# Kernel optimization log

Hardware: AMD Instinct MI355X
Metric: run time of the kernel (lower is better)

Reference implementation:

```python
import jax, jax.numpy as jnp
import numpy as np

GROUPS = 32
GN_EPS = 1e-6


def setup_inputs() -> dict:
    key = jax.random.key(0)
    ks = jax.random.split(key, 6)
    B, C, H, W = 2, 512, 64, 64
    s = 1.0 / np.sqrt(C)
    return {
        "x": jax.random.normal(ks[0], (B, C, H, W), jnp.float32),
        "gamma": jnp.ones((C,), jnp.float32),
        "beta": jnp.zeros((C,), jnp.float32),
        "wq": jax.random.normal(ks[1], (C, C), jnp.float32) * s,
        "bq": jnp.zeros((C,), jnp.float32),
        "wk": jax.random.normal(ks[2], (C, C), jnp.float32) * s,
        "bk": jnp.zeros((C,), jnp.float32),
        "wv": jax.random.normal(ks[3], (C, C), jnp.float32) * s,
        "bv": jnp.zeros((C,), jnp.float32),
        "wp": jax.random.normal(ks[4], (C, C), jnp.float32) * s,
        "bp": jnp.zeros((C,), jnp.float32),
    }


def _group_norm(x, gamma, beta):
    B, C, H, W = x.shape
    xg = x.reshape(B, GROUPS, C // GROUPS, H, W)
    mean = jnp.mean(xg, axis=(2, 3, 4), keepdims=True)
    var = jnp.mean(jnp.square(xg - mean), axis=(2, 3, 4), keepdims=True)
    xn = ((xg - mean) * jax.lax.rsqrt(var + GN_EPS)).reshape(B, C, H, W)
    return xn * gamma[None, :, None, None] + beta[None, :, None, None]


def _conv1x1(x, w, b):
    # 1x1 conv == per-pixel linear over channels; w: [out, in]
    return jnp.einsum('oc,bchw->bohw', w, x) + b[None, :, None, None]


def reference(x, gamma, beta, wq, bq, wk, bk, wv, bv, wp, bp):
    B, C, H, W = x.shape
    N = H * W
    h = _group_norm(x, gamma, beta)
    q = _conv1x1(h, wq, bq).reshape(B, C, N)  # [B, C, N]
    k = _conv1x1(h, wk, bk).reshape(B, C, N)
    v = _conv1x1(h, wv, bv).reshape(B, C, N)
    scale = C ** (-0.5)
    # attn[b, i, j] = softmax_j(q_i . k_j * scale)
    scores = jnp.einsum('bci,bcj->bij', q, k) * scale
    attn = jax.nn.softmax(scores, axis=2)
    # out[b, c, i] = sum_j attn[b, i, j] * v[b, c, j]
    o = jnp.einsum('bij,bcj->bci', attn, v).reshape(B, C, H, W)
    o = _conv1x1(o, wp, bp)
    return x + o
```

## Files before the change

kernel.cpp:

```cpp
#include <hip/hip_runtime.h>
#include <hip/hip_bf16.h>

using bf16 = __hip_bfloat16;
typedef __attribute__((ext_vector_type(4))) float f32x4;
typedef __attribute__((ext_vector_type(8))) short bf16x8;

#define NPX 4096
#define CCH 512

struct Ptr8 { void* p[8]; };

struct GemmP {
  const bf16* A; const bf16* B; void* C;
  const float* bias_m; const float* bias_n; const float* resid;
  float* rspart;
  float alpha; int K;
  int lda, ldb, ldc;
  long long sA, sB, sC, sR;
  int gx, gy;
  int omode;
};

__device__ __forceinline__ void async16(const bf16* g, bf16* l) {
  __builtin_amdgcn_global_load_lds((const __attribute__((address_space(1))) void*)g,
                                   (__attribute__((address_space(3))) void*)l, 16, 0, 0);
}

__device__ __forceinline__ float bfb2f(short s) {
  unsigned u = ((unsigned)(unsigned short)s) << 16;
  float f;
  __builtin_memcpy(&f, &u, 4);
  return f;
}

__device__ __forceinline__ short f2bfb(float f) {
  bf16 h = __float2bfloat16(f);
  short s;
  __builtin_memcpy(&s, &h, 2);
  return s;
}

__global__ __launch_bounds__(256) void prep_kernel(
    const float* __restrict__ wq, const float* __restrict__ wk,
    const float* __restrict__ wv, const float* __restrict__ wp,
    const float* __restrict__ bq, const float* __restrict__ bk,
    const float* __restrict__ x,
    bf16* __restrict__ wout, float* __restrict__ bqk, float* __restrict__ pstats) {
  int bid = blockIdx.x;
  int t = threadIdx.x;
  if (bid < 1024) {
    int tid = bid * 256 + t;
    int i = tid * 4;
    int seg = i >> 18;
    const float* in = seg == 0 ? wq : seg == 1 ? wk : seg == 2 ? wv : wp;
    float4 v = *reinterpret_cast<const float4*>(in + (i & 262143));
    wout[i]     = __float2bfloat16(v.x);
    wout[i + 1] = __float2bfloat16(v.y);
    wout[i + 2] = __float2bfloat16(v.z);
    wout[i + 3] = __float2bfloat16(v.w);
    if (tid < 256) {
      int j = tid * 4;
      const float* bsrc = j < 512 ? bq : bk;
      float4 b = *reinterpret_cast<const float4*>(bsrc + (j & 511));
      *reinterpret_cast<float4*>(bqk + j) = b;
    }
  } else {
    int bp = bid - 1024;
    const float* p = x + (size_t)bp * 8192;
    float s = 0.f, s2 = 0.f;
    #pragma unroll
    for (int j = 0; j < 8; j++) {
      float4 v = *reinterpret_cast<const float4*>(p + j * 1024 + t * 4);
      s  += v.x + v.y + v.z + v.w;
      s2 += v.x * v.x + v.y * v.y + v.z * v.z + v.w * v.w;
    }
    #pragma unroll
    for (int off = 32; off >= 1; off >>= 1) {
      s  += __shfl_xor(s, off);
      s2 += __shfl_xor(s2, off);
    }
    __shared__ float ls[8];
    int wv_ = t >> 6;
    if ((t & 63) == 0) { ls[wv_ * 2] = s; ls[wv_ * 2 + 1] = s2; }
    __syncthreads();
    if (t == 0) {
      pstats[bp * 2]     = ls[0] + ls[2] + ls[4] + ls[6];
      pstats[bp * 2 + 1] = ls[1] + ls[3] + ls[5] + ls[7];
    }
  }
}

__global__ __launch_bounds__(256) void gn_apply_kernel(const float* __restrict__ x,
    const float* __restrict__ pstats, const float* __restrict__ gamma,
    const float* __restrict__ beta, bf16* __restrict__ h) {
  __shared__ float tile[64][65];
  __shared__ float mr[4][2];
  int b  = blockIdx.z;
  int c0 = blockIdx.x * 64, n0 = blockIdx.y * 64;
  int t  = threadIdx.x;
  if (t < 4) {
    int g = (c0 >> 4) + t;
    float S = 0.f, S2 = 0.f;
    #pragma unroll
    for (int k2 = 0; k2 < 8; k2++) {
      S  += pstats[((b * 32 + g) * 8 + k2) * 2];
      S2 += pstats[((b * 32 + g) * 8 + k2) * 2 + 1];
    }
    float mean = S * (1.f / 65536.f);
    float var  = S2 * (1.f / 65536.f) - mean * mean;
    mr[t][0] = mean;
    mr[t][1] = rsqrtf(var + 1e-6f);
  }
  __syncthreads();
  int cl = t >> 6, nl = t & 63;
  #pragma unroll
  for (int i = 0; i < 16; i++) {
    int c = c0 + cl + i * 4;
    float v = x[((size_t)b * CCH + c) * NPX + n0 + nl];
    int gi = (cl + i * 4) >> 4;
    tile[cl + i * 4][nl] = (v - mr[gi][0]) * mr[gi][1] * gamma[c] + beta[c];
  }
  __syncthreads();
  #pragma unroll
  for (int i = 0; i < 16; i++) {
    int n = cl + i * 4;
    int c = nl;
    h[((size_t)b * NPX + n0 + n) * CCH + c0 + c] = __float2bfloat16(tile[c][n]);
  }
}

__global__ __launch_bounds__(256, 4) void gemm_any_kernel(GemmP p0, GemmP p1, unsigned nb0) {
  unsigned nwg = gridDim.x;
  unsigned flat = blockIdx.x;
  unsigned swz = (flat & 7) * (nwg >> 3) + (flat >> 3);
  GemmP p = swz < nb0 ? p0 : p1;
  unsigned local = swz < nb0 ? swz : swz - nb0;
  unsigned bxi = local % p.gx;
  unsigned tmp = local / p.gx;
  unsigned byi = tmp % p.gy;
  unsigned bz  = tmp / p.gy;

  const bf16* A = p.A + (size_t)bz * p.sA;
  const bf16* B = p.B + (size_t)bz * p.sB;
  const int m0 = bxi * 128, n0 = byi * 128;

  __shared__ bf16 ldsA[128 * 64];
  __shared__ bf16 ldsB[128 * 64];

  const int t = threadIdx.x;
  const int lane = t & 63, wv = t >> 6;
  const int wr = (wv >> 1) * 64, wc = (wv & 1) * 64;

  const int r0 = t >> 3;
  const int cb = ((t & 7) << 4) ^ ((r0 & 7) << 4);
  const bf16* gA = A + (size_t)(m0 + r0) * p.lda + (cb >> 1);
  const bf16* gB = B + (size_t)(n0 + r0) * p.ldb + (cb >> 1);
  bf16* lA = ldsA + t * 8;
  bf16* lB = ldsB + t * 8;

  const int arow = wr + (lane & 15);
  const int brow = wc + (lane & 15);
  const int kb   = (lane >> 4) * 16;

  f32x4 acc[4][4] = {};

  for (int k0 = 0; k0 < p.K; k0 += 64) {
    #pragma unroll
    for (int i = 0; i < 4; i++) {
      async16(gA + (size_t)i * 32 * p.lda + k0, lA + i * 2048);
      async16(gB + (size_t)i * 32 * p.ldb + k0, lB + i * 2048);
    }
    __syncthreads();
    #pragma unroll
    for (int ks = 0; ks < 2; ks++) {
      bf16x8 af[4], bfr[4];
      #pragma unroll
      for (int f = 0; f < 4; f++) {
        int ra = arow + f * 16;
        af[f] = *reinterpret_cast<const bf16x8*>(
            reinterpret_cast<const char*>(ldsA) + ra * 128 + ((ks * 64 + kb) ^ ((ra & 7) << 4)));
        int rb = brow + f * 16;
        bfr[f] = *reinterpret_cast<const bf16x8*>(
            reinterpret_cast<const char*>(ldsB) + rb * 128 + ((ks * 64 + kb) ^ ((rb & 7) << 4)));
      }
      #pragma unroll
      for (int fm = 0; fm < 4; fm++)
        #pragma unroll
        for (int fn = 0; fn < 4; fn++)
          acc[fm][fn] = __builtin_amdgcn_mfma_f32_16x16x32_bf16(af[fm], bfr[fn], acc[fm][fn], 0, 0, 0);
    }
    __syncthreads();
  }

  #pragma unroll
  for (int fm = 0; fm < 4; fm++) {
    #pragma unroll
    for (int j = 0; j < 4; j++) {
      int gm = m0 + wr + fm * 16 + (lane >> 4) * 4 + j;
      if (p.omode == 2) {
        float rsum = 0.f;
        #pragma unroll
        for (int fn = 0; fn < 4; fn++) {
          int gn = n0 + wc + fn * 16 + (lane & 15);
          float e = __expf(acc[fm][fn][j] * p.alpha);
          rsum += e;
          reinterpret_cast<bf16*>(p.C)[(size_t)bz * p.sC + (size_t)gm * p.ldc + gn] = __float2bfloat16(e);
        }
        rsum += __shfl_xor(rsum, 1);
        rsum += __shfl_xor(rsum, 2);
        rsum += __shfl_xor(rsum, 4);
        rsum += __shfl_xor(rsum, 8);
        if ((lane & 15) == 0)
          p.rspart[(((size_t)bz * 4096 + gm) << 6) + byi * 2 + (wv & 1)] = rsum;
      } else {
        float bm = p.bias_m ? p.bias_m[gm] : 0.f;
        #pragma unroll
        for (int fn = 0; fn < 4; fn++) {
          int gn = n0 + wc + fn * 16 + (lane & 15);
          float vv = acc[fm][fn][j] * p.alpha + bm;
          if (p.bias_n) vv += p.bias_n[gn];
          if (p.resid)  vv += p.resid[(size_t)bz * p.sR + (size_t)gm * p.ldc + gn];
          if (p.omode == 1)
            reinterpret_cast<bf16*>(p.C)[(size_t)bz * p.sC + (size_t)gm * p.ldc + gn] = __float2bfloat16(vv);
          else
            reinterpret_cast<float*>(p.C)[(size_t)bz * p.sC + (size_t)gm * p.ldc + gn] = vv;
        }
      }
    }
  }
}

__global__ __launch_bounds__(256, 4) void pv_split_kernel(
    const bf16* __restrict__ Sb, const bf16* __restrict__ vb,
    const float* __restrict__ rspart,
    long long sS, long long sV, Ptr8 slots, int mode) {
  unsigned nx = gridDim.x, ny = gridDim.y;
  unsigned flat = (blockIdx.z * ny + blockIdx.y) * nx + blockIdx.x;
  unsigned nwg = nx * ny * gridDim.z;
  unsigned swz = (flat & 7) * (nwg >> 3) + (flat >> 3);
  unsigned bxi = swz % nx;
  unsigned tmp = swz / nx;
  unsigned byi = tmp % ny;
  unsigned bz  = tmp / ny;

  const int z = bz;
  const int b = mode ? 0 : (z >> 2);
  const int s = mode ? z : (z & 3);
  const bf16* A = Sb + (size_t)b * sS + s * 1024;
  const bf16* B = vb + (size_t)b * sV + s * 1024;
  bf16* Cp = (bf16*)(slots.p[z]);
  const int m0 = bxi * 128, n0 = byi * 128;

  __shared__ bf16 ldsA[128 * 64];
  __shared__ bf16 ldsB[128 * 64];
  __shared__ float rs_lds[128];

  const int t = threadIdx.x;

  if (t < 128) {
    const float4* pp = reinterpret_cast<const float4*>(rspart + (((size_t)b * 4096 + m0 + t) << 6));
    float ssum = 0.f;
    #pragma unroll
    for (int i2 = 0; i2 < 16; i2++) {
      float4 vv = pp[i2];
      ssum += vv.x + vv.y + vv.z + vv.w;
    }
    rs_lds[t] = 1.0f / ssum;
  }

  const int lane = t & 63, wv = t >> 6;
  const int wr = (wv >> 1) * 64, wc = (wv & 1) * 64;

  const int r0 = t >> 3;
  const int cb = ((t & 7) << 4) ^ ((r0 & 7) << 4);
  const bf16* gA = A + (size_t)(m0 + r0) * 4096 + (cb >> 1);
  const bf16* gB = B + (size_t)(n0 + r0) * 4096 + (cb >> 1);
  bf16* lA = ldsA + t * 8;
  bf16* lB = ldsB + t * 8;

  const int arow = wr + (lane & 15);
  const int brow = wc + (lane & 15);
  const int kb   = (lane >> 4) * 16;

  f32x4 acc[4][4] = {};

  for (int k0 = 0; k0 < 1024; k0 += 64) {
    #pragma unroll
    for (int i = 0; i < 4; i++) {
      async16(gA + (size_t)i * 32 * 4096 + k0, lA + i * 2048);
      async16(gB + (size_t)i * 32 * 4096 + k0, lB + i * 2048);
    }
    __syncthreads();
    #pragma unroll
    for (int ks = 0; ks < 2; ks++) {
      bf16x8 af[4], bfr[4];
      #pragma unroll
      for (int f = 0; f < 4; f++) {
        int ra = arow + f * 16;
        af[f] = *reinterpret_cast<const bf16x8*>(
            reinterpret_cast<const char*>(ldsA) + ra * 128 + ((ks * 64 + kb) ^ ((ra & 7) << 4)));
        int rb = brow + f * 16;
        bfr[f] = *reinterpret_cast<const bf16x8*>(
            reinterpret_cast<const char*>(ldsB) + rb * 128 + ((ks * 64 + kb) ^ ((rb & 7) << 4)));
      }
      #pragma unroll
      for (int fm = 0; fm < 4; fm++)
        #pragma unroll
        for (int fn = 0; fn < 4; fn++)
          acc[fm][fn] = __builtin_amdgcn_mfma_f32_16x16x32_bf16(af[fm], bfr[fn], acc[fm][fn], 0, 0, 0);
    }
    __syncthreads();
  }

  #pragma unroll
  for (int fm = 0; fm < 4; fm++) {
    #pragma unroll
    for (int j = 0; j < 4; j++) {
      int lrow = wr + fm * 16 + (lane >> 4) * 4 + j;
      float inv = rs_lds[lrow];
      int gm = m0 + lrow;
      #pragma unroll
      for (int fn = 0; fn < 4; fn++) {
        int gn = n0 + wc + fn * 16 + (lane & 15);
        Cp[(size_t)gm * 512 + gn] = __float2bfloat16(acc[fm][fn][j] * inv);
      }
    }
  }
}

__global__ __launch_bounds__(256) void reduce3_kernel(bf16* __restrict__ dst,
    const bf16* __restrict__ p1, const bf16* __restrict__ p2,
    const bf16* __restrict__ p3) {
  int i = (blockIdx.x * 256 + threadIdx.x) * 8;
  bf16x8 a  = *reinterpret_cast<const bf16x8*>(dst + i);
  bf16x8 v1 = *reinterpret_cast<const bf16x8*>(p1 + i);
  bf16x8 v2 = *reinterpret_cast<const bf16x8*>(p2 + i);
  bf16x8 v3 = *reinterpret_cast<const bf16x8*>(p3 + i);
  bf16x8 r;
  #pragma unroll
  for (int j = 0; j < 8; j++)
    r[j] = f2bfb(bfb2f(a[j]) + bfb2f(v1[j]) + bfb2f(v2[j]) + bfb2f(v3[j]));
  *reinterpret_cast<bf16x8*>(dst + i) = r;
}

extern "C" void kernel_launch(void* const* d_in, const int* in_sizes, int n_in,
                              void* d_out, int out_size, void* d_ws, size_t ws_size,
                              hipStream_t stream) {
  const float* x     = (const float*)d_in[0];
  const float* gamma = (const float*)d_in[1];
  const float* beta  = (const float*)d_in[2];
  const float* wq    = (const float*)d_in[3];
  const float* bq    = (const float*)d_in[4];
  const float* wk    = (const float*)d_in[5];
  const float* bk    = (const float*)d_in[6];
  const float* wv    = (const float*)d_in[7];
  const float* bv    = (const float*)d_in[8];
  const float* wp    = (const float*)d_in[9];
  const float* bp    = (const float*)d_in[10];
  float* out = (float*)d_out;

  char* w = (char*)d_ws;
  size_t off = 0;
  float* pstats = (float*)(w + off);   off += 4096;
  float* bqk    = (float*)(w + off);   off += 4096;
  float* rspart = (float*)(w + off);   off += (size_t)2 * 4096 * 64 * 4;
  bf16* wqkb = (bf16*)(w + off);       off += (size_t)1024 * 512 * 2;
  bf16* wvb  = (bf16*)(w + off);       off += (size_t)512 * 512 * 2;
  bf16* wpb  = (bf16*)(w + off);       off += (size_t)512 * 512 * 2;
  bf16* h    = (bf16*)(w + off);       off += (size_t)2 * NPX * CCH * 2;
  bf16* qk   = (bf16*)(w + off);       off += (size_t)2 * NPX * 1024 * 2;
  bf16* v    = (bf16*)(w + off);       off += (size_t)2 * NPX * CCH * 2;
  bf16* o    = (bf16*)(w + off);       off += (size_t)2 * NPX * CCH * 2;
  bf16* S    = (bf16*)(w + off);
  size_t need_big = off + (size_t)2 * NPX * NPX * 2;
  const bool big = ws_size >= need_big;

  const long long sBN = (long long)NPX * CCH;
  const long long sQK = (long long)NPX * 1024;
  const long long sS  = (long long)NPX * NPX;
  const float scale = 0.04419417382415922f;

  prep_kernel<<<1536, 256, 0, stream>>>(wq, wk, wv, wp, bq, bk, x, wqkb, bqk, pstats);
  gn_apply_kernel<<<dim3(8, 64, 2), 256, 0, stream>>>(x, pstats, gamma, beta, h);

  GemmP pqkv = {h, wqkb, qk, nullptr, bqk, nullptr, nullptr,
                1.f, 512, 512, 512, 1024, sBN, 0, sQK, 0, 32, 8, 1};
  GemmP pv   = {wvb, h, v, bv, nullptr, nullptr, nullptr,
                1.f, 512, 512, 512, 4096, 0, sBN, sBN, 0, 4, 32, 1};
  gemm_any_kernel<<<768, 256, 0, stream>>>(pqkv, pv, 512);

  if (big) {
    GemmP ps = {qk, qk + 512, S, nullptr, nullptr, nullptr, rspart,
                scale, 512, 1024, 1024, 4096, sQK, sQK, sS, 0, 32, 32, 2};
    gemm_any_kernel<<<2048, 256, 0, stream>>>(ps, ps, 2048);
    Ptr8 slots{{o, h, qk, qk + sBN, o + sBN, h + sBN, qk + 2 * sBN, qk + 3 * sBN}};
    pv_split_kernel<<<dim3(32, 4, 8), 256, 0, stream>>>(S, v, rspart, sS, sBN, slots, 0);
    reduce3_kernel<<<1024, 256, 0, stream>>>(o, h, qk, qk + sBN);
    reduce3_kernel<<<1024, 256, 0, stream>>>(o + sBN, h + sBN, qk + 2 * sBN, qk + 3 * sBN);
  } else {
    for (int b = 0; b < 2; b++) {
      GemmP ps = {qk + b * sQK, qk + b * sQK + 512, S, nullptr, nullptr, nullptr,
                  rspart + ((size_t)b << 18),
                  scale, 512, 1024, 1024, 4096, 0, 0, 0, 0, 32, 32, 2};
      gemm_any_kernel<<<1024, 256, 0, stream>>>(ps, ps, 1024);
      Ptr8 slots{{o + b * sBN, h, h + sBN, (bf16*)out, nullptr, nullptr, nullptr, nullptr}};
      pv_split_kernel<<<dim3(32, 4, 4), 256, 0, stream>>>(S, v + b * sBN,
          rspart + ((size_t)b << 18), 0, 0, slots, 1);
      reduce3_kernel<<<1024, 256, 0, stream>>>(o + b * sBN, h, h + sBN, (bf16*)out);
    }
  }

  GemmP po = {wpb, o, out, bp, nullptr, x, nullptr,
              1.f, 512, 512, 512, 4096, 0, sBN, sBN, sBN, 4, 32, 0};
  gemm_any_kernel<<<256, 256, 0, stream>>>(po, po, 256);
}
```

Baseline: 268.7 us.

## Add 256x256 ping-pong pipelined PV split kernel and merge reduce launches

Replaces the PV split-K GEMM, which used 128-ish tiles, with a new 512-thread kernel computing 256x256 output tiles. It double-buffers LDS with async global-to-LDS loads, uses an XOR-swizzled layout, interleaves MFMA phases with explicit waitcnt, barriers and setprio, and uses a grid swizzle. The two per-batch reduce launches are also merged into one kernel. The goal is more data reuse per tile and overlap of memory loads with MFMA work, at the cost of one workgroup per CU and heavy hand-written scheduling.

Result: faster. 254.8 us (-5.2%).

```diff
diff --git a/kernel.cpp b/kernel.cpp
--- a/kernel.cpp
+++ b/kernel.cpp
@@ -230,6 +230,149 @@
   }
 }
 
+#define BAR() __builtin_amdgcn_s_barrier()
+#define LGKM0() do { asm volatile("s_waitcnt lgkmcnt(0)" ::: "memory"); \
+                     __builtin_amdgcn_sched_barrier(0); } while (0)
+#define VMC2() do { asm volatile("s_waitcnt vmcnt(2)" ::: "memory"); \
+                    __builtin_amdgcn_sched_barrier(0); } while (0)
+#define VMC0() do { asm volatile("s_waitcnt vmcnt(0)" ::: "memory"); \
+                    __builtin_amdgcn_sched_barrier(0); } while (0)
+
+#define STG(op, buf, half, kt) do { \
+    const bf16* _s = (op ? gB : gA) + (size_t)((half) * 128) * 4096 + (kt) * 64; \
+    bf16* _d = &lds[op][buf][half][t * 8]; \
+    async16(_s, _d); \
+    async16(_s + (size_t)64 * 4096, _d + 4096); \
+  } while (0)
+
+#define DSA(buf, mrb) do { \
+    _Pragma("unroll") \
+    for (int mi = 0; mi < 4; mi++) { \
+      int _r = ((mrb) + mi) * 16 + (l & 15); \
+      _Pragma("unroll") \
+      for (int ks = 0; ks < 2; ks++) \
+        aR[mi][ks] = *reinterpret_cast<const bf16x8*>( \
+            &lds[0][buf][wm][_r * 64 + ((ks * 32 + (l >> 4) * 8) ^ ((l & 7) << 3))]); \
+    } } while (0)
+
+#define DSB(buf, nrb) do { \
+    _Pragma("unroll") \
+    for (int ni = 0; ni < 2; ni++) { \
+      int _r = (wn & 1) * 64 + ((nrb) + ni) * 16 + (l & 15); \
+      _Pragma("unroll") \
+      for (int ks = 0; ks < 2; ks++) \
+        bR[ni][ks] = *reinterpret_cast<const bf16x8*>( \
+            &lds[1][buf][wn >> 1][_r * 64 + ((ks * 32 + (l >> 4) * 8) ^ ((l & 7) << 3))]); \
+    } } while (0)
+
+#define MMAQ(qm, qn) do { \
+    _Pragma("unroll") \
+    for (int mi = 0; mi < 4; mi++) \
+    _Pragma("unroll") \
+    for (int ni = 0; ni < 2; ni++) \
+    _Pragma("unroll") \
+    for (int ks = 0; ks < 2; ks++) \
+      acc[(qm) * 4 + mi][(qn) * 2 + ni] = __builtin_amdgcn_mfma_f32_16x16x32_bf16( \
+          aR[mi][ks], bR[ni][ks], acc[(qm) * 4 + mi][(qn) * 2 + ni], 0, 0, 0); \
+  } while (0)
+
+#define PH_TAIL(qm, qn) do { \
+    BAR(); LGKM0(); \
+    __builtin_amdgcn_s_setprio(1); MMAQ(qm, qn); __builtin_amdgcn_s_setprio(0); \
+    BAR(); } while (0)
+
+__global__ __launch_bounds__(512, 1) void pv8_kernel(
+    const bf16* __restrict__ Sb, const bf16* __restrict__ vb,
+    const float* __restrict__ rspart, Ptr8 slots) {
+  unsigned nwg = gridDim.x;
+  unsigned flat = blockIdx.x;
+  unsigned swz = (flat & 7) * (nwg >> 3) + (flat >> 3);
+  const unsigned zz = swz >> 5;
+  const unsigned tile = swz & 31;
+  const int m0 = (tile & 15) * 256;
+  const int n0 = (tile >> 4) * 256;
+  const int b = zz >> 2, s = zz & 3;
+  const bf16* A = Sb + (size_t)b * 16777216 + s * 1024;
+  const bf16* B = vb + (size_t)b * 2097152 + s * 1024;
+  bf16* Cp = (bf16*)(slots.p[zz]);
+
+  __shared__ bf16 lds[2][2][2][8192];
+  __shared__ float rs_lds[256];
+
+  const int t = threadIdx.x;
+  const int l = t & 63;
+  const int wid = t >> 6;
+  const int wm = wid >> 2;
+  const int wn = wid & 3;
+
+  const int swzc = (((t & 7) ^ ((t >> 3) & 7)) << 3);
+  const bf16* gA = A + (size_t)(m0 + (t >> 3)) * 4096 + swzc;
+  const bf16* gB = B + (size_t)(n0 + (t >> 3)) * 4096 + swzc;
+
+  f32x4 acc[8][4] = {};
+  bf16x8 aR[4][2], bR[2][2];
+
+  STG(0, 0, 0, 0);
+  STG(0, 0, 1, 0);
+  STG(1, 0, 0, 0);
+  STG(1, 0, 1, 0);
+  STG(1, 1, 0, 1);
+  VMC0();
+  BAR();
+
+  #pragma unroll 1
+  for (int j = 0; j < 7; j++) {
+    const int kt1 = 2 * j + 1, kt2 = 2 * j + 2, kt3 = 2 * j + 3;
+    DSA(0, 0); DSB(0, 0); STG(1, 1, 1, kt1); PH_TAIL(0, 0);
+    DSA(0, 4);            STG(0, 1, 0, kt1); PH_TAIL(1, 0);
+    DSB(0, 2);            STG(0, 1, 1, kt1); PH_TAIL(1, 1);
+    DSA(0, 0);            STG(1, 0, 0, kt2); VMC2(); PH_TAIL(0, 1);
+    DSA(1, 0); DSB(1, 0); STG(1, 0, 1, kt2); PH_TAIL(0, 0);
+    DSA(1, 4);            STG(0, 0, 0, kt2); PH_TAIL(1, 0);
+    DSB(1, 2);            STG(0, 0, 1, kt2); PH_TAIL(1, 1);
+    DSA(1, 0);            STG(1, 1, 0, kt3); VMC2(); PH_TAIL(0, 1);
+  }
+  {
+    const int kt1 = 15;
+    DSA(0, 0); DSB(0, 0); STG(1, 1, 1, kt1); PH_TAIL(0, 0);
+    DSA(0, 4);            STG(0, 1, 0, kt1); PH_TAIL(1, 0);
+    DSB(0, 2);            STG(0, 1, 1, kt1); PH_TAIL(1, 1);
+    DSA(0, 0);            VMC0(); PH_TAIL(0, 1);
+    DSA(1, 0); DSB(1, 0); PH_TAIL(0, 0);
+    DSA(1, 4);            PH_TAIL(1, 0);
+    DSB(1, 2);            PH_TAIL(1, 1);
+    DSA(1, 0);            PH_TAIL(0, 1);
+  }
+
+  if (t < 256) {
+    const float4* pp = reinterpret_cast<const float4*>(
+        rspart + (((size_t)b * 4096 + m0 + t) << 6));
+    float ssum = 0.f;
+    #pragma unroll
+    for (int i2 = 0; i2 < 16; i2++) {
+      float4 vv = pp[i2];
+      ssum += vv.x + vv.y + vv.z + vv.w;
+    }
+    rs_lds[t] = 1.0f / ssum;
+  }
+  __syncthreads();
+
+  #pragma unroll
+  for (int mr = 0; mr < 8; mr++) {
+    #pragma unroll
+    for (int jj = 0; jj < 4; jj++) {
+      int lrow = wm * 128 + mr * 16 + (l >> 4) * 4 + jj;
+      float inv = rs_lds[lrow];
+      int gm = m0 + lrow;
+      #pragma unroll
+      for (int nr = 0; nr < 4; nr++) {
+        int gn = n0 + wn * 64 + nr * 16 + (l & 15);
+        Cp[(size_t)gm * 512 + gn] = __float2bfloat16(acc[mr][nr][jj] * inv);
+      }
+    }
+  }
+}
+
 __global__ __launch_bounds__(256, 4) void pv_split_kernel(
     const bf16* __restrict__ Sb, const bf16* __restrict__ vb,
     const float* __restrict__ rspart,
@@ -328,6 +471,26 @@
   }
 }
 
+__global__ __launch_bounds__(256) void reduce3x2_kernel(bf16* __restrict__ o,
+    const bf16* __restrict__ h, const bf16* __restrict__ qk) {
+  int i = (blockIdx.x * 256 + threadIdx.x) * 8;
+  int b = i >> 21;
+  int ii = i & 2097151;
+  bf16* dst = o + (size_t)b * 2097152 + ii;
+  const bf16* p1 = h + (size_t)b * 2097152 + ii;
+  const bf16* p2 = qk + (size_t)b * 2 * 2097152 + ii;
+  const bf16* p3 = qk + (size_t)(b * 2 + 1) * 2097152 + ii;
+  bf16x8 a  = *reinterpret_cast<const bf16x8*>(dst);
+  bf16x8 v1 = *reinterpret_cast<const bf16x8*>(p1);
+  bf16x8 v2 = *reinterpret_cast<const bf16x8*>(p2);
+  bf16x8 v3 = *reinterpret_cast<const bf16x8*>(p3);
+  bf16x8 r;
+  #pragma unroll
+  for (int j = 0; j < 8; j++)
+    r[j] = f2bfb(bfb2f(a[j]) + bfb2f(v1[j]) + bfb2f(v2[j]) + bfb2f(v3[j]));
+  *reinterpret_cast<bf16x8*>(dst) = r;
+}
+
 __global__ __launch_bounds__(256) void reduce3_kernel(bf16* __restrict__ dst,
     const bf16* __restrict__ p1, const bf16* __restrict__ p2,
     const bf16* __restrict__ p3) {
@@ -394,9 +557,8 @@
                 scale, 512, 1024, 1024, 4096, sQK, sQK, sS, 0, 32, 32, 2};
     gemm_any_kernel<<<2048, 256, 0, stream>>>(ps, ps, 2048);
     Ptr8 slots{{o, h, qk, qk + sBN, o + sBN, h + sBN, qk + 2 * sBN, qk + 3 * sBN}};
-    pv_split_kernel<<<dim3(32, 4, 8), 256, 0, stream>>>(S, v, rspart, sS, sBN, slots, 0);
-    reduce3_kernel<<<1024, 256, 0, stream>>>(o, h, qk, qk + sBN);
-    reduce3_kernel<<<1024, 256, 0, stream>>>(o + sBN, h + sBN, qk + 2 * sBN, qk + 3 * sBN);
+    pv8_kernel<<<256, 512, 0, stream>>>(S, v, rspart, slots);
+    reduce3x2_kernel<<<2048, 256, 0, stream>>>(o, h, qk);
   } else {
     for (int b = 0; b < 2; b++) {
       GemmP ps = {qk + b * sQK, qk + b * sQK + 512, S, nullptr, nullptr, nullptr,
```
